# Performance work log

Hardware: AMD Instinct MI355X
Metric: run time of the kernel (lower is better)

## Reference

```python
import jax, jax.numpy as jnp
import numpy as np

B, N, E = 32, 128, 16384
D, H, O, A = 72, 72, 72, 4   # n_input, n_hidden, n_output, n_node_attr
C_WEIGHT = 1.0
EPS = 1e-5  # BatchNorm1d default eps


def setup_inputs() -> dict:
    key = jax.random.key(0)
    ks = jax.random.split(key, 16)
    rn = lambda k, shp, s=0.05: jax.random.normal(k, shp, jnp.float32) * s
    return {
        "h": jax.random.normal(ks[0], (B, N, D), jnp.float32),
        "x": jax.random.normal(ks[1], (B, N, 4), jnp.float32),
        "edgei": jax.random.randint(ks[2], (B, E), 0, N),
        "edgej": jax.random.randint(ks[3], (B, E), 0, N),
        "node_attr": jax.random.normal(ks[4], (B, N, A), jnp.float32),
        # phi_e: Linear(2D+2 -> H, no bias), BN, ReLU, Linear(H->H), ReLU
        "We1": rn(ks[5], (2 * D + 2, H)),
        "g1": jnp.ones((H,), jnp.float32), "b1": jnp.zeros((H,), jnp.float32),
        "We2": rn(ks[6], (H, H)), "be2": jnp.zeros((H,), jnp.float32),
        # phi_m: Linear(H->1), Sigmoid
        "Wm": rn(ks[7], (H, 1)), "bm": jnp.zeros((1,), jnp.float32),
        # phi_x: Linear(H->H), ReLU, Linear(H->1, no bias, tiny init)
        "Wx1": rn(ks[8], (H, H)), "bx1": jnp.zeros((H,), jnp.float32),
        "Wx2": rn(ks[9], (H, 1), 0.001),
        # phi_h: Linear(H+D+A -> H), BN, ReLU, Linear(H->O)
        "Wh1": rn(ks[10], (H + D + A, H)), "bh1": jnp.zeros((H,), jnp.float32),
        "gh": jnp.ones((H,), jnp.float32), "bh": jnp.zeros((H,), jnp.float32),
        "Wh2": rn(ks[11], (H, O)), "bh2": jnp.zeros((O,), jnp.float32),
    }


def _psi(p):
    return jnp.sign(p) * jnp.log1p(jnp.abs(p))


def _normsq4(p):  # Minkowski norm: p0^2 - p1^2 - p2^2 - p3^2
    psq = p * p
    return 2.0 * psq[..., 0] - psq.sum(axis=-1)


def _dotsq4(p, q):  # Minkowski inner product
    pq = p * q
    return 2.0 * pq[..., 0] - pq.sum(axis=-1)


def _batchnorm(z, g, b):  # training-mode BatchNorm1d over flattened batch dim
    mu = z.mean(axis=0)
    var = z.var(axis=0)
    return (z - mu) * jax.lax.rsqrt(var + EPS) * g + b


_seg_sum = jax.vmap(lambda d, s: jax.ops.segment_sum(d, s, num_segments=N))


def reference(h, x, edgei, edgej, node_attr,
              We1, g1, b1, We2, be2, Wm, bm,
              Wx1, bx1, Wx2, Wh1, bh1, gh, bh, Wh2, bh2):
    # gather edge endpoint features (equiv. to torch.gather along dim 1)
    xi = jnp.take_along_axis(x, edgei[:, :, None], axis=1)    # [B,E,4]
    xj = jnp.take_along_axis(x, edgej[:, :, None], axis=1)
    hi = jnp.take_along_axis(h, edgei[:, :, None], axis=1)    # [B,E,D]
    hj = jnp.take_along_axis(h, edgej[:, :, None], axis=1)
    x_diff = xi - xj
    norms = _psi(_normsq4(x_diff))[..., None]                 # [B,E,1]
    dots = _psi(_dotsq4(xi, xj))[..., None]                   # [B,E,1]

    # m_model: phi_e then sigmoid gate phi_m
    feat = jnp.concatenate([hi, hj, norms, dots], axis=-1)    # [B,E,2D+2]
    z = feat.reshape(-1, 2 * D + 2) @ We1
    z = jax.nn.relu(_batchnorm(z, g1, b1))
    z = jax.nn.relu(z @ We2 + be2)
    m = z.reshape(B, E, H)
    m = m * jax.nn.sigmoid(m @ Wm + bm)                       # gated messages

    # x_model: equivariant coordinate update (segment mean over edges)
    gate = jax.nn.relu(m @ Wx1 + bx1) @ Wx2                   # [B,E,1]
    trans = jnp.clip(x_diff * gate, -100.0, 100.0)
    agg = _seg_sum(trans, edgei)                              # [B,N,4]
    cnt = _seg_sum(jnp.ones_like(trans), edgei)
    x_out = x + (agg / jnp.maximum(cnt, 1.0)) * C_WEIGHT

    # h_model: segment sum of messages, node MLP, residual
    magg = _seg_sum(m, edgei)                                 # [B,N,H]
    hin = jnp.concatenate([h, magg, node_attr], axis=-1).reshape(-1, H + D + A)
    z2 = hin @ Wh1 + bh1
    z2 = jax.nn.relu(_batchnorm(z2, gh, bh))
    z2 = z2 @ Wh2 + bh2
    h_out = h + z2.reshape(B, N, O)

    return (h_out, x_out, m)
```

## Files before the change

### kernel.cpp

```cpp
#include <hip/hip_runtime.h>

#define BB 32
#define NN 128
#define EE 16384
#define ROWS_E (BB*EE)
#define ROWS_N (BB*NN)
#define EPS_BN 1e-5f

#define XOUT_OFF (ROWS_N*72)
#define M_OFF    (XOUT_OFF + ROWS_N*4)

#define ST1_OFF 0
#define ST2_OFF 512
#define AGG_OFF 1024
#define CNT_OFF (AGG_OFF + ROWS_N*4)
#define MAGG_OFF (CNT_OFF + ROWS_N)
#define Z2_OFF (MAGG_OFF + ROWS_N*72)
#define ZERO_FLOATS Z2_OFF
#define WB_OFF (Z2_OFF + ROWS_N*72)

#define WE1T_OFF 0
#define WE2T_OFF 13440
#define WX1T_OFF 21760
#define WH1T_OFF 30080
#define WH2T_OFF 43520
#define WB_TOTAL 51840

#define SS 168

typedef __attribute__((ext_vector_type(8))) short short8;
typedef __attribute__((ext_vector_type(4))) float f32x4;

__device__ __forceinline__ float psi_f(float p) {
    return copysignf(log1pf(fabsf(p)), p);
}
__device__ __forceinline__ unsigned pk(float a, float b) {
    unsigned r;
    asm("v_cvt_pk_bf16_f32 %0, %1, %2" : "=v"(r) : "v"(a), "v"(b));
    return r;
}
__device__ __forceinline__ unsigned short f2bf(float f) {
    unsigned r;
    asm("v_cvt_pk_bf16_f32 %0, %1, %1" : "=v"(r) : "v"(f));
    return (unsigned short)r;
}

__global__ void k_prep(const float* __restrict__ We1, const float* __restrict__ We2,
                       const float* __restrict__ Wx1, const float* __restrict__ Wh1,
                       const float* __restrict__ Wh2, unsigned short* __restrict__ wb)
{
    int idx = blockIdx.x * 256 + threadIdx.x;
    if (idx >= WB_TOTAL) return;
    const float* src; int off, n, k, K;
    if (idx < WE2T_OFF)      { off = idx;            n = off/168; k = off%168; src = We1; K = 146; }
    else if (idx < WH1T_OFF && idx >= WX1T_OFF) { off = idx - WX1T_OFF; n = off/104; k = off%104; src = Wx1; K = 72; }
    else if (idx < WX1T_OFF) { off = idx - WE2T_OFF; n = off/104; k = off%104; src = We2; K = 72; }
    else if (idx < WH2T_OFF) { off = idx - WH1T_OFF; n = off/168; k = off%168; src = Wh1; K = 148; }
    else                     { off = idx - WH2T_OFF; n = off/104; k = off%104; src = Wh2; K = 72; }
    float v = (n < 72 && k < K) ? src[k * 72 + n] : 0.f;
    wb[idx] = f2bf(v);
}

__device__ __forceinline__ void stage_feat(
    unsigned short* At, const float* __restrict__ h, const float* __restrict__ x,
    const int* __restrict__ ei, const int* __restrict__ ej, int tid, int blk)
{
    int rl = tid >> 1, half = tid & 1;
    int row = blk * 128 + rl;
    int b = row >> 14;
    int i = ei[row], j = ej[row];
    int node = half ? j : i;
    const float4* hp = (const float4*)(h + (size_t)(b * 128 + node) * 72);
    uint2* arow = (uint2*)(&At[rl * SS + half * 72]);
    #pragma unroll
    for (int q = 0; q < 18; q++) {
        float4 v = hp[q];
        arow[q] = make_uint2(pk(v.x, v.y), pk(v.z, v.w));
    }
    if (half == 0) {
        float4 xi = *(const float4*)(x + (size_t)(b * 128 + i) * 4);
        float4 xj = *(const float4*)(x + (size_t)(b * 128 + j) * 4);
        float d0 = xi.x - xj.x, d1 = xi.y - xj.y, d2 = xi.z - xj.z, d3 = xi.w - xj.w;
        float nrm = d0*d0 - d1*d1 - d2*d2 - d3*d3;
        float dot = xi.x*xj.x - xi.y*xj.y - xi.z*xj.z - xi.w*xj.w;
        *(unsigned*)(&At[rl * SS + 144]) = pk(psi_f(nrm), psi_f(dot));
        unsigned* tp = (unsigned*)(&At[rl * SS + 146]);
        tp[0] = 0u; tp[1] = 0u; tp[2] = 0u;
    } else {
        unsigned* tp = (unsigned*)(&At[rl * SS + 152]);
        tp[0] = 0u; tp[1] = 0u; tp[2] = 0u; tp[3] = 0u;
    }
}

__global__ __launch_bounds__(256, 3) void k_edge_stats(
    const float* __restrict__ h, const float* __restrict__ x,
    const int* __restrict__ ei, const int* __restrict__ ej,
    const unsigned short* __restrict__ We1t, float* __restrict__ st)
{
    __shared__ unsigned short At[128 * SS];
    int tid = threadIdx.x;
    stage_feat(At, h, x, ei, ej, tid, blockIdx.x);

    int wv = tid >> 6, lane = tid & 63, c = lane & 15, quad = lane >> 4;
    f32x4 acc[2][5] = {};
    for (int kc = 0; kc < 5; kc++) {
        int k0 = kc * 32 + quad * 8;
        short8 a0 = *(const short8*)(&At[(wv * 32 + c) * SS + k0]);
        short8 a1 = *(const short8*)(&At[(wv * 32 + 16 + c) * SS + k0]);
        #pragma unroll
        for (int ct = 0; ct < 5; ct++) {
            short8 bf = *(const short8*)(&We1t[(ct * 16 + c) * 168 + k0]);
            acc[0][ct] = __builtin_amdgcn_mfma_f32_16x16x32_bf16(a0, bf, acc[0][ct], 0, 0, 0);
            acc[1][ct] = __builtin_amdgcn_mfma_f32_16x16x32_bf16(a1, bf, acc[1][ct], 0, 0, 0);
        }
    }
    float* sredw = (float*)(&At[wv * 32 * SS]);
    #pragma unroll
    for (int ct = 0; ct < 5; ct++) {
        int col = ct * 16 + c;
        float s = 0.f, q = 0.f;
        #pragma unroll
        for (int rt = 0; rt < 2; rt++)
            #pragma unroll
            for (int r = 0; r < 4; r++) {
                float v = acc[rt][ct][r];
                s += v; q += v * v;
            }
        s += __shfl_xor(s, 16); s += __shfl_xor(s, 32);
        q += __shfl_xor(q, 16); q += __shfl_xor(q, 32);
        if (lane < 16 && col < 72) { sredw[col] = s; sredw[72 + col] = q; }
    }
    __syncthreads();
    if (tid < 144) {
        const float* a = (const float*)At;
        atomicAdd(&st[tid], a[tid] + a[2688 + tid] + a[5376 + tid] + a[8064 + tid]);
    }
}

__global__ void k_finalize(float* __restrict__ st, float inv_rows)
{
    int c = threadIdx.x;
    if (c < 72) {
        float mean = st[c] * inv_rows;
        float var  = st[72 + c] * inv_rows - mean * mean;
        st[144 + c] = mean;
        st[216 + c] = rsqrtf(var + EPS_BN);
    }
}

__global__ __launch_bounds__(256, 3) void k_edge_fused(
    const float* __restrict__ h, const float* __restrict__ x,
    const int* __restrict__ ei, const int* __restrict__ ej,
    const float* __restrict__ st1, const float* __restrict__ g1, const float* __restrict__ b1,
    const float* __restrict__ be2, const float* __restrict__ Wm, const float* __restrict__ bm,
    const float* __restrict__ bx1, const float* __restrict__ Wx2,
    const unsigned short* __restrict__ We1t, const unsigned short* __restrict__ We2t,
    const unsigned short* __restrict__ Wx1t,
    float* __restrict__ m, float* __restrict__ agg, float* __restrict__ cnt)
{
    __shared__ unsigned short At[128 * SS];
    int tid = threadIdx.x;
    stage_feat(At, h, x, ei, ej, tid, blockIdx.x);

    int wv = tid >> 6, lane = tid & 63, c = lane & 15, quad = lane >> 4;
    f32x4 acc1[2][5] = {};
    for (int kc = 0; kc < 5; kc++) {
        int k0 = kc * 32 + quad * 8;
        short8 a0 = *(const short8*)(&At[(wv * 32 + c) * SS + k0]);
        short8 a1 = *(const short8*)(&At[(wv * 32 + 16 + c) * SS + k0]);
        #pragma unroll
        for (int ct = 0; ct < 5; ct++) {
            short8 bf = *(const short8*)(&We1t[(ct * 16 + c) * 168 + k0]);
            acc1[0][ct] = __builtin_amdgcn_mfma_f32_16x16x32_bf16(a0, bf, acc1[0][ct], 0, 0, 0);
            acc1[1][ct] = __builtin_amdgcn_mfma_f32_16x16x32_bf16(a1, bf, acc1[1][ct], 0, 0, 0);
        }
    }
    const float* mean = st1 + 144;
    const float* inv  = st1 + 216;
    #pragma unroll
    for (int ct = 0; ct < 5; ct++) {
        int col = ct * 16 + c;
        float mu = 0.f, iv = 0.f, ga = 0.f, be = 0.f;
        if (col < 72) { mu = mean[col]; iv = inv[col]; ga = g1[col]; be = b1[col]; }
        #pragma unroll
        for (int rt = 0; rt < 2; rt++)
            #pragma unroll
            for (int r = 0; r < 4; r++) {
                float a = (col < 72) ? fmaxf((acc1[rt][ct][r] - mu) * iv * ga + be, 0.f) : 0.f;
                int lrow = wv * 32 + rt * 16 + quad * 4 + r;
                At[lrow * SS + col] = f2bf(a);
            }
    }
    {
        int r_ = lane >> 1, h_ = lane & 1;
        uint* zp = (uint*)&At[(wv * 32 + r_) * SS + 80 + h_ * 8];
        zp[0] = 0u; zp[1] = 0u; zp[2] = 0u; zp[3] = 0u;
    }
    f32x4 acc2[2][5] = {};
    for (int kc = 0; kc < 3; kc++) {
        int k0 = kc * 32 + quad * 8;
        short8 a0 = *(const short8*)(&At[(wv * 32 + c) * SS + k0]);
        short8 a1 = *(const short8*)(&At[(wv * 32 + 16 + c) * SS + k0]);
        #pragma unroll
        for (int ct = 0; ct < 5; ct++) {
            short8 bf = *(const short8*)(&We2t[(ct * 16 + c) * 104 + k0]);
            acc2[0][ct] = __builtin_amdgcn_mfma_f32_16x16x32_bf16(a0, bf, acc2[0][ct], 0, 0, 0);
            acc2[1][ct] = __builtin_amdgcn_mfma_f32_16x16x32_bf16(a1, bf, acc2[1][ct], 0, 0, 0);
        }
    }
    float part[2][4] = {};
    float bm0 = bm[0];
    #pragma unroll
    for (int ct = 0; ct < 5; ct++) {
        int col = ct * 16 + c;
        float bias = (col < 72) ? be2[col] : 0.f;
        float wm   = (col < 72) ? Wm[col]  : 0.f;
        #pragma unroll
        for (int rt = 0; rt < 2; rt++)
            #pragma unroll
            for (int r = 0; r < 4; r++) {
                float t = fmaxf(acc2[rt][ct][r] + bias, 0.f);
                acc2[rt][ct][r] = t;
                part[rt][r] += t * wm;
            }
    }
    float sg[2][4];
    #pragma unroll
    for (int rt = 0; rt < 2; rt++)
        #pragma unroll
        for (int r = 0; r < 4; r++) {
            float s = part[rt][r];
            s += __shfl_xor(s, 1); s += __shfl_xor(s, 2);
            s += __shfl_xor(s, 4); s += __shfl_xor(s, 8);
            sg[rt][r] = 1.f / (1.f + expf(-(s + bm0)));
        }
    size_t rbase = (size_t)blockIdx.x * 128 + wv * 32 + quad * 4;
    #pragma unroll
    for (int rt = 0; rt < 2; rt++)
        #pragma unroll
        for (int ct = 0; ct < 5; ct++) {
            int col = ct * 16 + c;
            #pragma unroll
            for (int r = 0; r < 4; r++) {
                float mv = acc2[rt][ct][r] * sg[rt][r];
                int lrow = wv * 32 + rt * 16 + quad * 4 + r;
                At[lrow * SS + col] = f2bf(mv);
                if (col < 72) m[(rbase + rt * 16 + r) * 72 + col] = mv;
            }
        }
    f32x4 acc3[2][5] = {};
    for (int kc = 0; kc < 3; kc++) {
        int k0 = kc * 32 + quad * 8;
        short8 a0 = *(const short8*)(&At[(wv * 32 + c) * SS + k0]);
        short8 a1 = *(const short8*)(&At[(wv * 32 + 16 + c) * SS + k0]);
        #pragma unroll
        for (int ct = 0; ct < 5; ct++) {
            short8 bf = *(const short8*)(&Wx1t[(ct * 16 + c) * 104 + k0]);
            acc3[0][ct] = __builtin_amdgcn_mfma_f32_16x16x32_bf16(a0, bf, acc3[0][ct], 0, 0, 0);
            acc3[1][ct] = __builtin_amdgcn_mfma_f32_16x16x32_bf16(a1, bf, acc3[1][ct], 0, 0, 0);
        }
    }
    float part3[2][4] = {};
    #pragma unroll
    for (int ct = 0; ct < 5; ct++) {
        int col = ct * 16 + c;
        float bias = (col < 72) ? bx1[col] : 0.f;
        float wx   = (col < 72) ? Wx2[col] : 0.f;
        #pragma unroll
        for (int rt = 0; rt < 2; rt++)
            #pragma unroll
            for (int r = 0; r < 4; r++)
                part3[rt][r] += fmaxf(acc3[rt][ct][r] + bias, 0.f) * wx;
    }
    float* gp = (float*)&At[(wv * 32) * SS + 96];
    #pragma unroll
    for (int rt = 0; rt < 2; rt++)
        #pragma unroll
        for (int r = 0; r < 4; r++) {
            float s = part3[rt][r];
            s += __shfl_xor(s, 1); s += __shfl_xor(s, 2);
            s += __shfl_xor(s, 4); s += __shfl_xor(s, 8);
            if (c == 0) gp[rt * 16 + quad * 4 + r] = s;
        }
    __syncthreads();
    if (tid < 128) {
        size_t erow = (size_t)blockIdx.x * 128 + tid;
        int b = (int)(erow >> 14);
        int i2 = ei[erow], j2 = ej[erow];
        float g2 = *((float*)&At[((tid >> 5) * 32) * SS + 96] + (tid & 31));
        float4 xi = *(const float4*)(x + (size_t)(b * 128 + i2) * 4);
        float4 xj = *(const float4*)(x + (size_t)(b * 128 + j2) * 4);
        float t0 = fminf(fmaxf((xi.x - xj.x) * g2, -100.f), 100.f);
        float t1 = fminf(fmaxf((xi.y - xj.y) * g2, -100.f), 100.f);
        float t2 = fminf(fmaxf((xi.z - xj.z) * g2, -100.f), 100.f);
        float t3 = fminf(fmaxf((xi.w - xj.w) * g2, -100.f), 100.f);
        float* ap = agg + (size_t)(b * 128 + i2) * 4;
        atomicAdd(ap + 0, t0); atomicAdd(ap + 1, t1);
        atomicAdd(ap + 2, t2); atomicAdd(ap + 3, t3);
        atomicAdd(cnt + (size_t)(b * 128 + i2), 1.f);
    }
}

__global__ __launch_bounds__(256, 4) void k_magg(
    const float* __restrict__ m, const int* __restrict__ ei, float* __restrict__ magg)
{
    __shared__ float accum[128 * 72];
    int tid = threadIdx.x;
    for (int q = tid; q < 9216; q += 256) accum[q] = 0.f;
    __syncthreads();
    int b = blockIdx.x >> 5, chunk = blockIdx.x & 31;
    int wv = tid >> 6, lane = tid & 63;
    int ebase = b * 16384 + chunk * 512;
    for (int e = wv; e < 512; e += 8) {
        int e0 = ebase + e, e1 = ebase + e + 4;
        int n0 = ei[e0], n1 = ei[e1];
        const float* r0 = m + (size_t)e0 * 72;
        const float* r1 = m + (size_t)e1 * 72;
        float v0 = r0[lane];
        float v1 = r1[lane];
        float t0 = (lane < 8) ? r0[64 + lane] : 0.f;
        float t1 = (lane < 8) ? r1[64 + lane] : 0.f;
        atomicAdd(&accum[n0 * 72 + lane], v0);
        if (lane < 8) atomicAdd(&accum[n0 * 72 + 64 + lane], t0);
        atomicAdd(&accum[n1 * 72 + lane], v1);
        if (lane < 8) atomicAdd(&accum[n1 * 72 + 64 + lane], t1);
    }
    __syncthreads();
    float* mg = magg + (size_t)b * 9216;
    for (int q = tid; q < 9216; q += 256) atomicAdd(&mg[q], accum[q]);
}

__global__ __launch_bounds__(256) void k_node_gemm1(
    const float* __restrict__ h, const float* __restrict__ node_attr,
    const float* __restrict__ magg, const unsigned short* __restrict__ Wh1t,
    const float* __restrict__ bh1, float* __restrict__ z2, float* __restrict__ st)
{
    __shared__ unsigned short At[128 * 168];
    __shared__ unsigned short Wt[80 * 168];
    __shared__ float sred[4][144];
    int tid = threadIdx.x;
    {
        const uint4* s = (const uint4*)Wh1t; uint4* d = (uint4*)Wt;
        for (int q = tid; q < 1680; q += 256) d[q] = s[q];
    }
    int rl = tid >> 1, half = tid & 1;
    size_t row = (size_t)blockIdx.x * 128 + rl;
    const float4* sp = (const float4*)((half ? magg : h) + row * 72);
    uint2* arow = (uint2*)(&At[rl * 168 + half * 72]);
    #pragma unroll
    for (int q = 0; q < 18; q++) {
        float4 v = sp[q];
        arow[q] = make_uint2(pk(v.x, v.y), pk(v.z, v.w));
    }
    if (half) {
        float4 na = *(const float4*)(node_attr + row * 4);
        *(unsigned*)(&At[rl * 168 + 144]) = pk(na.x, na.y);
        *(unsigned*)(&At[rl * 168 + 146]) = pk(na.z, na.w);
        unsigned* tailp = (unsigned*)(&At[rl * 168 + 148]);
        #pragma unroll
        for (int q = 0; q < 10; q++) tailp[q] = 0u;
    }
    __syncthreads();

    int wv = tid >> 6, lane = tid & 63, c = lane & 15, quad = lane >> 4;
    f32x4 acc[2][5] = {};
    for (int kc = 0; kc < 5; kc++) {
        int k0 = kc * 32 + quad * 8;
        short8 a0 = *(const short8*)(&At[(wv * 32 + c) * 168 + k0]);
        short8 a1 = *(const short8*)(&At[(wv * 32 + 16 + c) * 168 + k0]);
        #pragma unroll
        for (int ct = 0; ct < 5; ct++) {
            short8 bf = *(const short8*)(&Wt[(ct * 16 + c) * 168 + k0]);
            acc[0][ct] = __builtin_amdgcn_mfma_f32_16x16x32_bf16(a0, bf, acc[0][ct], 0, 0, 0);
            acc[1][ct] = __builtin_amdgcn_mfma_f32_16x16x32_bf16(a1, bf, acc[1][ct], 0, 0, 0);
        }
    }
    size_t rbase = (size_t)blockIdx.x * 128 + wv * 32 + quad * 4;
    #pragma unroll
    for (int ct = 0; ct < 5; ct++) {
        int col = ct * 16 + c;
        float bias = (col < 72) ? bh1[col] : 0.f;
        float s = 0.f, q = 0.f;
        #pragma unroll
        for (int rt = 0; rt < 2; rt++) {
            float* op = z2 + (rbase + rt * 16) * 72 + col;
            #pragma unroll
            for (int r = 0; r < 4; r++) {
                float v = acc[rt][ct][r] + bias;
                if (col < 72) op[(size_t)r * 72] = v;
                s += v; q += v * v;
            }
        }
        s += __shfl_xor(s, 16); s += __shfl_xor(s, 32);
        q += __shfl_xor(q, 16); q += __shfl_xor(q, 32);
        if (lane < 16 && col < 72) { sred[wv][col] = s; sred[wv][72 + col] = q; }
    }
    __syncthreads();
    if (tid < 144)
        atomicAdd(&st[tid], sred[0][tid] + sred[1][tid] + sred[2][tid] + sred[3][tid]);
}

__global__ __launch_bounds__(256) void k_node_final(
    const float* __restrict__ h, const float* __restrict__ x,
    const float* __restrict__ z2, const float* __restrict__ st2,
    const float* __restrict__ gh, const float* __restrict__ bh,
    const unsigned short* __restrict__ Wh2t, const float* __restrict__ bh2,
    const float* __restrict__ agg, const float* __restrict__ cnt,
    float* __restrict__ hout, float* __restrict__ xout)
{
    __shared__ unsigned short Zt[128 * 104];
    __shared__ unsigned short Wt[80 * 104];
    int tid = threadIdx.x;
    {
        const uint4* s = (const uint4*)Wh2t; uint4* d = (uint4*)Wt;
        for (int q = tid; q < 1040; q += 256) d[q] = s[q];
    }
    int rl = tid >> 1, half = tid & 1;
    size_t row = (size_t)blockIdx.x * 128 + rl;
    const float* mean = st2 + 144;
    const float* inv  = st2 + 216;
    const float4* zp = (const float4*)(z2 + row * 72) + half * 9;
    uint2* arow = (uint2*)(&Zt[rl * 104 + half * 36]);
    #pragma unroll
    for (int q = 0; q < 9; q++) {
        int k = half * 36 + q * 4;
        float4 v = zp[q];
        float a0 = fmaxf((v.x - mean[k  ]) * inv[k  ] * gh[k  ] + bh[k  ], 0.f);
        float a1 = fmaxf((v.y - mean[k+1]) * inv[k+1] * gh[k+1] + bh[k+1], 0.f);
        float a2 = fmaxf((v.z - mean[k+2]) * inv[k+2] * gh[k+2] + bh[k+2], 0.f);
        float a3 = fmaxf((v.w - mean[k+3]) * inv[k+3] * gh[k+3] + bh[k+3], 0.f);
        arow[q] = make_uint2(pk(a0, a1), pk(a2, a3));
    }
    uint2* prow = (uint2*)(&Zt[rl * 104]);
    #pragma unroll
    for (int q = 0; q < 4; q++) prow[18 + half * 4 + q] = make_uint2(0u, 0u);
    __syncthreads();

    int wv = tid >> 6, lane = tid & 63, c = lane & 15, quad = lane >> 4;
    f32x4 acc[2][5] = {};
    for (int kc = 0; kc < 3; kc++) {
        int k0 = kc * 32 + quad * 8;
        short8 a0 = *(const short8*)(&Zt[(wv * 32 + c) * 104 + k0]);
        short8 a1 = *(const short8*)(&Zt[(wv * 32 + 16 + c) * 104 + k0]);
        #pragma unroll
        for (int ct = 0; ct < 5; ct++) {
            short8 bf = *(const short8*)(&Wt[(ct * 16 + c) * 104 + k0]);
            acc[0][ct] = __builtin_amdgcn_mfma_f32_16x16x32_bf16(a0, bf, acc[0][ct], 0, 0, 0);
            acc[1][ct] = __builtin_amdgcn_mfma_f32_16x16x32_bf16(a1, bf, acc[1][ct], 0, 0, 0);
        }
    }
    size_t rbase = (size_t)blockIdx.x * 128 + wv * 32 + quad * 4;
    #pragma unroll
    for (int rt = 0; rt < 2; rt++)
        #pragma unroll
        for (int ct = 0; ct < 5; ct++) {
            int col = ct * 16 + c;
            if (col < 72) {
                float bias = bh2[col];
                #pragma unroll
                for (int r = 0; r < 4; r++) {
                    size_t gr = (rbase + rt * 16 + r);
                    hout[gr * 72 + col] = h[gr * 72 + col] + acc[rt][ct][r] + bias;
                }
            }
        }
    if (tid < 128) {
        size_t nrow = (size_t)blockIdx.x * 128 + tid;
        float cn = fmaxf(cnt[nrow], 1.f);
        float4 ag = *(const float4*)(agg + nrow * 4);
        float4 xv = *(const float4*)(x + nrow * 4);
        ((float4*)xout)[nrow] = make_float4(xv.x + ag.x / cn, xv.y + ag.y / cn,
                                            xv.z + ag.z / cn, xv.w + ag.w / cn);
    }
}

extern "C" void kernel_launch(void* const* d_in, const int* in_sizes, int n_in,
                              void* d_out, int out_size, void* d_ws, size_t ws_size,
                              hipStream_t stream)
{
    const float* h   = (const float*)d_in[0];
    const float* x   = (const float*)d_in[1];
    const int*   ei  = (const int*)d_in[2];
    const int*   ej  = (const int*)d_in[3];
    const float* na  = (const float*)d_in[4];
    const float* We1 = (const float*)d_in[5];
    const float* g1  = (const float*)d_in[6];
    const float* b1  = (const float*)d_in[7];
    const float* We2 = (const float*)d_in[8];
    const float* be2 = (const float*)d_in[9];
    const float* Wm  = (const float*)d_in[10];
    const float* bm  = (const float*)d_in[11];
    const float* Wx1 = (const float*)d_in[12];
    const float* bx1 = (const float*)d_in[13];
    const float* Wx2 = (const float*)d_in[14];
    const float* Wh1 = (const float*)d_in[15];
    const float* bh1 = (const float*)d_in[16];
    const float* gh  = (const float*)d_in[17];
    const float* bhp = (const float*)d_in[18];
    const float* Wh2 = (const float*)d_in[19];
    const float* bh2 = (const float*)d_in[20];

    float* out  = (float*)d_out;
    float* hout = out;
    float* xout = out + XOUT_OFF;
    float* m    = out + M_OFF;
    float* ws   = (float*)d_ws;
    float* st1  = ws + ST1_OFF;
    float* st2  = ws + ST2_OFF;
    float* agg  = ws + AGG_OFF;
    float* cnt  = ws + CNT_OFF;
    float* magg = ws + MAGG_OFF;
    float* z2   = ws + Z2_OFF;
    unsigned short* wb = (unsigned short*)(ws + WB_OFF);

    hipMemsetAsync(d_ws, 0, (size_t)ZERO_FLOATS * sizeof(float), stream);
    k_prep<<<(WB_TOTAL + 255) / 256, 256, 0, stream>>>(We1, We2, Wx1, Wh1, Wh2, wb);
    k_edge_stats<<<ROWS_E / 128, 256, 0, stream>>>(h, x, ei, ej, wb + WE1T_OFF, st1);
    k_finalize<<<1, 128, 0, stream>>>(st1, 1.0f / (float)ROWS_E);
    k_edge_fused<<<ROWS_E / 128, 256, 0, stream>>>(h, x, ei, ej, st1, g1, b1, be2, Wm, bm,
                                                   bx1, Wx2, wb + WE1T_OFF, wb + WE2T_OFF,
                                                   wb + WX1T_OFF, m, agg, cnt);
    k_magg<<<1024, 256, 0, stream>>>(m, ei, magg);
    k_node_gemm1<<<ROWS_N / 128, 256, 0, stream>>>(h, na, magg, wb + WH1T_OFF, bh1, z2, st2);
    k_finalize<<<1, 128, 0, stream>>>(st2, 1.0f / (float)ROWS_N);
    k_node_final<<<ROWS_N / 128, 256, 0, stream>>>(h, x, z2, st2, gh, bhp,
                                                   wb + WH2T_OFF, bh2, agg, cnt, hout, xout);
}
```

Measured before the change: 700.1 us.

## Factor first edge linear layer into per-node projections gathered per edge

The first edge GEMM over concatenated [hi, hj, norms, dots] is split algebraically into per-node products h@We1[:72] and h@We1[72:144]. These are computed once per node (4096 rows instead of 524288 edges) and gathered per edge with the scalar terms added. The BN statistics pass becomes a lightweight gather-and-reduce kernel instead of a full MFMA pass, and the fused edge kernel skips its first GEMM. BN scale and shift are also prefolded into one multiply-add. It reuses workspace and the x_out buffer as scratch, which adds memset ordering dependencies, and it adds fp32 gathers of 144-wide node rows per edge.

```diff
diff --git a/kernel.cpp b/kernel.cpp
--- a/kernel.cpp
+++ b/kernel.cpp
@@ -16,7 +16,6 @@
 #define CNT_OFF (AGG_OFF + ROWS_N*4)
 #define MAGG_OFF (CNT_OFF + ROWS_N)
 #define Z2_OFF (MAGG_OFF + ROWS_N*72)
-#define ZERO_FLOATS Z2_OFF
 #define WB_OFF (Z2_OFF + ROWS_N*72)
 
 #define WE1T_OFF 0
@@ -25,8 +24,8 @@
 #define WH1T_OFF 30080
 #define WH2T_OFF 43520
 #define WB_TOTAL 51840
-
-#define SS 168
+#define WAB_TOTAL 13824
+#define PREP_TOTAL (WB_TOTAL + WAB_TOTAL)
 
 typedef __attribute__((ext_vector_type(8))) short short8;
 typedef __attribute__((ext_vector_type(4))) float f32x4;
@@ -47,10 +46,18 @@
 
 __global__ void k_prep(const float* __restrict__ We1, const float* __restrict__ We2,
                        const float* __restrict__ Wx1, const float* __restrict__ Wh1,
-                       const float* __restrict__ Wh2, unsigned short* __restrict__ wb)
+                       const float* __restrict__ Wh2, unsigned short* __restrict__ wb,
+                       unsigned short* __restrict__ wab)
 {
     int idx = blockIdx.x * 256 + threadIdx.x;
-    if (idx >= WB_TOTAL) return;
+    if (idx >= PREP_TOTAL) return;
+    if (idx >= WB_TOTAL) {
+        int off = idx - WB_TOTAL, n = off / 96, k = off % 96;
+        float v = 0.f;
+        if (k < 72) v = (n < 72) ? We1[k * 72 + n] : We1[(72 + k) * 72 + (n - 72)];
+        wab[off] = f2bf(v);
+        return;
+    }
     const float* src; int off, n, k, K;
     if (idx < WE2T_OFF)      { off = idx;            n = off/168; k = off%168; src = We1; K = 146; }
     else if (idx < WH1T_OFF && idx >= WX1T_OFF) { off = idx - WX1T_OFF; n = off/104; k = off%104; src = Wx1; K = 72; }
@@ -61,79 +68,94 @@
     wb[idx] = f2bf(v);
 }
 
-__device__ __forceinline__ void stage_feat(
-    unsigned short* At, const float* __restrict__ h, const float* __restrict__ x,
-    const int* __restrict__ ei, const int* __restrict__ ej, int tid, int blk)
-{
+__global__ __launch_bounds__(256, 2) void k_ab(
+    const float* __restrict__ h, const unsigned short* __restrict__ Wabt,
+    float* __restrict__ ab)
+{
+    __shared__ unsigned short Hs[128 * 104];
+    int tid = threadIdx.x;
     int rl = tid >> 1, half = tid & 1;
-    int row = blk * 128 + rl;
-    int b = row >> 14;
-    int i = ei[row], j = ej[row];
-    int node = half ? j : i;
-    const float4* hp = (const float4*)(h + (size_t)(b * 128 + node) * 72);
-    uint2* arow = (uint2*)(&At[rl * SS + half * 72]);
-    #pragma unroll
-    for (int q = 0; q < 18; q++) {
+    size_t row = (size_t)blockIdx.x * 128 + rl;
+    const float4* hp = (const float4*)(h + row * 72) + half * 9;
+    uint2* hr = (uint2*)(&Hs[rl * 104 + half * 36]);
+    #pragma unroll
+    for (int q = 0; q < 9; q++) {
         float4 v = hp[q];
-        arow[q] = make_uint2(pk(v.x, v.y), pk(v.z, v.w));
-    }
-    if (half == 0) {
+        hr[q] = make_uint2(pk(v.x, v.y), pk(v.z, v.w));
+    }
+    {
+        uint2* zp = (uint2*)(&Hs[rl * 104 + 72 + half * 12]);
+        zp[0] = make_uint2(0u, 0u); zp[1] = make_uint2(0u, 0u); zp[2] = make_uint2(0u, 0u);
+    }
+    int wv = tid >> 6, lane = tid & 63, c = lane & 15, quad = lane >> 4;
+    f32x4 acc[2][9] = {};
+    #pragma unroll
+    for (int kc = 0; kc < 3; kc++) {
+        int k0 = kc * 32 + quad * 8;
+        short8 a0 = *(const short8*)(&Hs[(wv * 32 + c) * 104 + k0]);
+        short8 a1 = *(const short8*)(&Hs[(wv * 32 + 16 + c) * 104 + k0]);
+        #pragma unroll
+        for (int ct = 0; ct < 9; ct++) {
+            short8 bf = *(const short8*)(&Wabt[(ct * 16 + c) * 96 + k0]);
+            acc[0][ct] = __builtin_amdgcn_mfma_f32_16x16x32_bf16(a0, bf, acc[0][ct], 0, 0, 0);
+            acc[1][ct] = __builtin_amdgcn_mfma_f32_16x16x32_bf16(a1, bf, acc[1][ct], 0, 0, 0);
+        }
+    }
+    size_t rbase = (size_t)blockIdx.x * 128 + wv * 32 + quad * 4;
+    #pragma unroll
+    for (int rt = 0; rt < 2; rt++)
+        #pragma unroll
+        for (int ct = 0; ct < 9; ct++) {
+            int col = ct * 16 + c;
+            #pragma unroll
+            for (int r = 0; r < 4; r++)
+                ab[(rbase + rt * 16 + r) * 144 + col] = acc[rt][ct][r];
+        }
+}
+
+__global__ void k_stats_lite(
+    const float* __restrict__ ab, const float* __restrict__ x,
+    const int* __restrict__ ei, const int* __restrict__ ej,
+    const float* __restrict__ We1, float* __restrict__ st)
+{
+    __shared__ float ssum[4][72];
+    __shared__ float ssq[4][72];
+    int c = threadIdx.x, ty = threadIdx.y;
+    float al = We1[144 * 72 + c], be = We1[145 * 72 + c];
+    float s = 0.f, q = 0.f;
+    for (int e = blockIdx.x * 4 + ty; e < ROWS_E; e += 4096) {
+        int b = e >> 14;
+        int i = ei[e], j = ej[e];
         float4 xi = *(const float4*)(x + (size_t)(b * 128 + i) * 4);
         float4 xj = *(const float4*)(x + (size_t)(b * 128 + j) * 4);
         float d0 = xi.x - xj.x, d1 = xi.y - xj.y, d2 = xi.z - xj.z, d3 = xi.w - xj.w;
-        float nrm = d0*d0 - d1*d1 - d2*d2 - d3*d3;
-        float dot = xi.x*xj.x - xi.y*xj.y - xi.z*xj.z - xi.w*xj.w;
-        *(unsigned*)(&At[rl * SS + 144]) = pk(psi_f(nrm), psi_f(dot));
-        unsigned* tp = (unsigned*)(&At[rl * SS + 146]);
-        tp[0] = 0u; tp[1] = 0u; tp[2] = 0u;
-    } else {
-        unsigned* tp = (unsigned*)(&At[rl * SS + 152]);
-        tp[0] = 0u; tp[1] = 0u; tp[2] = 0u; tp[3] = 0u;
-    }
-}
-
-__global__ __launch_bounds__(256, 3) void k_edge_stats(
-    const float* __restrict__ h, const float* __restrict__ x,
-    const int* __restrict__ ei, const int* __restrict__ ej,
-    const unsigned short* __restrict__ We1t, float* __restrict__ st)
-{
-    __shared__ unsigned short At[128 * SS];
-    int tid = threadIdx.x;
-    stage_feat(At, h, x, ei, ej, tid, blockIdx.x);
-
-    int wv = tid >> 6, lane = tid & 63, c = lane & 15, quad = lane >> 4;
-    f32x4 acc[2][5] = {};
-    for (int kc = 0; kc < 5; kc++) {
-        int k0 = kc * 32 + quad * 8;
-        short8 a0 = *(const short8*)(&At[(wv * 32 + c) * SS + k0]);
-        short8 a1 = *(const short8*)(&At[(wv * 32 + 16 + c) * SS + k0]);
-        #pragma unroll
-        for (int ct = 0; ct < 5; ct++) {
-            short8 bf = *(const short8*)(&We1t[(ct * 16 + c) * 168 + k0]);
-            acc[0][ct] = __builtin_amdgcn_mfma_f32_16x16x32_bf16(a0, bf, acc[0][ct], 0, 0, 0);
-            acc[1][ct] = __builtin_amdgcn_mfma_f32_16x16x32_bf16(a1, bf, acc[1][ct], 0, 0, 0);
-        }
-    }
-    float* sredw = (float*)(&At[wv * 32 * SS]);
-    #pragma unroll
-    for (int ct = 0; ct < 5; ct++) {
-        int col = ct * 16 + c;
-        float s = 0.f, q = 0.f;
-        #pragma unroll
-        for (int rt = 0; rt < 2; rt++)
-            #pragma unroll
-            for (int r = 0; r < 4; r++) {
-                float v = acc[rt][ct][r];
-                s += v; q += v * v;
-            }
-        s += __shfl_xor(s, 16); s += __shfl_xor(s, 32);
-        q += __shfl_xor(q, 16); q += __shfl_xor(q, 32);
-        if (lane < 16 && col < 72) { sredw[col] = s; sredw[72 + col] = q; }
-    }
-    __syncthreads();
-    if (tid < 144) {
-        const float* a = (const float*)At;
-        atomicAdd(&st[tid], a[tid] + a[2688 + tid] + a[5376 + tid] + a[8064 + tid]);
+        float u = psi_f(d0*d0 - d1*d1 - d2*d2 - d3*d3);
+        float t = psi_f(xi.x*xj.x - xi.y*xj.y - xi.z*xj.z - xi.w*xj.w);
+        float av = ab[(size_t)(b * 128 + i) * 144 + c];
+        float bv = ab[(size_t)(b * 128 + j) * 144 + 72 + c];
+        float z = av + bv + u * al + t * be;
+        s += z; q += z * z;
+    }
+    ssum[ty][c] = s; ssq[ty][c] = q;
+    __syncthreads();
+    if (ty == 0) {
+        s = ssum[0][c] + ssum[1][c] + ssum[2][c] + ssum[3][c];
+        q = ssq[0][c] + ssq[1][c] + ssq[2][c] + ssq[3][c];
+        atomicAdd(&st[c], s);
+        atomicAdd(&st[72 + c], q);
+    }
+}
+
+__global__ void k_finalize1(float* __restrict__ st, const float* __restrict__ g1,
+                            const float* __restrict__ b1, float inv_rows)
+{
+    int c = threadIdx.x;
+    if (c < 72) {
+        float mean = st[c] * inv_rows;
+        float var  = st[72 + c] * inv_rows - mean * mean;
+        float sc = rsqrtf(var + EPS_BN) * g1[c];
+        st[144 + c] = sc;
+        st[216 + c] = b1[c] - mean * sc;
     }
 }
 
@@ -148,59 +170,55 @@
     }
 }
 
-__global__ __launch_bounds__(256, 3) void k_edge_fused(
-    const float* __restrict__ h, const float* __restrict__ x,
+__global__ __launch_bounds__(256, 4) void k_edge_fused(
+    const float* __restrict__ ab, const float* __restrict__ x,
     const int* __restrict__ ei, const int* __restrict__ ej,
-    const float* __restrict__ st1, const float* __restrict__ g1, const float* __restrict__ b1,
+    const float* __restrict__ We1, const float* __restrict__ st1,
     const float* __restrict__ be2, const float* __restrict__ Wm, const float* __restrict__ bm,
     const float* __restrict__ bx1, const float* __restrict__ Wx2,
-    const unsigned short* __restrict__ We1t, const unsigned short* __restrict__ We2t,
-    const unsigned short* __restrict__ Wx1t,
+    const unsigned short* __restrict__ We2t, const unsigned short* __restrict__ Wx1t,
     float* __restrict__ m, float* __restrict__ agg, float* __restrict__ cnt)
 {
-    __shared__ unsigned short At[128 * SS];
+    __shared__ unsigned short Zt[128 * 104];
+    __shared__ float g2buf[128];
     int tid = threadIdx.x;
-    stage_feat(At, h, x, ei, ej, tid, blockIdx.x);
+    int rl = tid >> 1, half = tid & 1;
+    size_t row = (size_t)blockIdx.x * 128 + rl;
+    int b = (int)(row >> 14);
+    int i = ei[row], j = ej[row];
+    float4 xi = *(const float4*)(x + (size_t)(b * 128 + i) * 4);
+    float4 xj = *(const float4*)(x + (size_t)(b * 128 + j) * 4);
+    float d0 = xi.x - xj.x, d1 = xi.y - xj.y, d2 = xi.z - xj.z, d3 = xi.w - xj.w;
+    float u = psi_f(d0*d0 - d1*d1 - d2*d2 - d3*d3);
+    float t = psi_f(xi.x*xj.x - xi.y*xj.y - xi.z*xj.z - xi.w*xj.w);
+    const float4* ar  = (const float4*)(ab + (size_t)(b * 128 + i) * 144 + half * 36);
+    const float4* br  = (const float4*)(ab + (size_t)(b * 128 + j) * 144 + 72 + half * 36);
+    const float4* alp = (const float4*)(We1 + 144 * 72 + half * 36);
+    const float4* bep = (const float4*)(We1 + 145 * 72 + half * 36);
+    const float4* scp = (const float4*)(st1 + 144 + half * 36);
+    const float4* shp = (const float4*)(st1 + 216 + half * 36);
+    uint2* zrow = (uint2*)(&Zt[rl * 104 + half * 36]);
+    #pragma unroll
+    for (int q = 0; q < 9; q++) {
+        float4 av = ar[q], bv = br[q], al = alp[q], be = bep[q], sc = scp[q], sh = shp[q];
+        float z0 = fmaxf((av.x + bv.x + u * al.x + t * be.x) * sc.x + sh.x, 0.f);
+        float z1 = fmaxf((av.y + bv.y + u * al.y + t * be.y) * sc.y + sh.y, 0.f);
+        float z2 = fmaxf((av.z + bv.z + u * al.z + t * be.z) * sc.z + sh.z, 0.f);
+        float z3 = fmaxf((av.w + bv.w + u * al.w + t * be.w) * sc.w + sh.w, 0.f);
+        zrow[q] = make_uint2(pk(z0, z1), pk(z2, z3));
+    }
+    {
+        uint2* zp = (uint2*)(&Zt[rl * 104 + 72 + half * 12]);
+        zp[0] = make_uint2(0u, 0u); zp[1] = make_uint2(0u, 0u); zp[2] = make_uint2(0u, 0u);
+    }
 
     int wv = tid >> 6, lane = tid & 63, c = lane & 15, quad = lane >> 4;
-    f32x4 acc1[2][5] = {};
-    for (int kc = 0; kc < 5; kc++) {
-        int k0 = kc * 32 + quad * 8;
-        short8 a0 = *(const short8*)(&At[(wv * 32 + c) * SS + k0]);
-        short8 a1 = *(const short8*)(&At[(wv * 32 + 16 + c) * SS + k0]);
-        #pragma unroll
-        for (int ct = 0; ct < 5; ct++) {
-            short8 bf = *(const short8*)(&We1t[(ct * 16 + c) * 168 + k0]);
-            acc1[0][ct] = __builtin_amdgcn_mfma_f32_16x16x32_bf16(a0, bf, acc1[0][ct], 0, 0, 0);
-            acc1[1][ct] = __builtin_amdgcn_mfma_f32_16x16x32_bf16(a1, bf, acc1[1][ct], 0, 0, 0);
-        }
-    }
-    const float* mean = st1 + 144;
-    const float* inv  = st1 + 216;
-    #pragma unroll
-    for (int ct = 0; ct < 5; ct++) {
-        int col = ct * 16 + c;
-        float mu = 0.f, iv = 0.f, ga = 0.f, be = 0.f;
-        if (col < 72) { mu = mean[col]; iv = inv[col]; ga = g1[col]; be = b1[col]; }
-        #pragma unroll
-        for (int rt = 0; rt < 2; rt++)
-            #pragma unroll
-            for (int r = 0; r < 4; r++) {
-                float a = (col < 72) ? fmaxf((acc1[rt][ct][r] - mu) * iv * ga + be, 0.f) : 0.f;
-                int lrow = wv * 32 + rt * 16 + quad * 4 + r;
-                At[lrow * SS + col] = f2bf(a);
-            }
-    }
-    {
-        int r_ = lane >> 1, h_ = lane & 1;
-        uint* zp = (uint*)&At[(wv * 32 + r_) * SS + 80 + h_ * 8];
-        zp[0] = 0u; zp[1] = 0u; zp[2] = 0u; zp[3] = 0u;
-    }
     f32x4 acc2[2][5] = {};
+    #pragma unroll
     for (int kc = 0; kc < 3; kc++) {
         int k0 = kc * 32 + quad * 8;
-        short8 a0 = *(const short8*)(&At[(wv * 32 + c) * SS + k0]);
-        short8 a1 = *(const short8*)(&At[(wv * 32 + 16 + c) * SS + k0]);
+        short8 a0 = *(const short8*)(&Zt[(wv * 32 + c) * 104 + k0]);
+        short8 a1 = *(const short8*)(&Zt[(wv * 32 + 16 + c) * 104 + k0]);
         #pragma unroll
         for (int ct = 0; ct < 5; ct++) {
             short8 bf = *(const short8*)(&We2t[(ct * 16 + c) * 104 + k0]);
@@ -219,9 +237,9 @@
         for (int rt = 0; rt < 2; rt++)
             #pragma unroll
             for (int r = 0; r < 4; r++) {
-                float t = fmaxf(acc2[rt][ct][r] + bias, 0.f);
-                acc2[rt][ct][r] = t;
-                part[rt][r] += t * wm;
+                float tv = fmaxf(acc2[rt][ct][r] + bias, 0.f);
+                acc2[rt][ct][r] = tv;
+                part[rt][r] += tv * wm;
             }
     }
     float sg[2][4];
@@ -244,15 +262,16 @@
             for (int r = 0; r < 4; r++) {
                 float mv = acc2[rt][ct][r] * sg[rt][r];
                 int lrow = wv * 32 + rt * 16 + quad * 4 + r;
-                At[lrow * SS + col] = f2bf(mv);
+                Zt[lrow * 104 + col] = f2bf(mv);
                 if (col < 72) m[(rbase + rt * 16 + r) * 72 + col] = mv;
             }
         }
     f32x4 acc3[2][5] = {};
+    #pragma unroll
     for (int kc = 0; kc < 3; kc++) {
         int k0 = kc * 32 + quad * 8;
-        short8 a0 = *(const short8*)(&At[(wv * 32 + c) * SS + k0]);
-        short8 a1 = *(const short8*)(&At[(wv * 32 + 16 + c) * SS + k0]);
+        short8 a0 = *(const short8*)(&Zt[(wv * 32 + c) * 104 + k0]);
+        short8 a1 = *(const short8*)(&Zt[(wv * 32 + 16 + c) * 104 + k0]);
         #pragma unroll
         for (int ct = 0; ct < 5; ct++) {
             short8 bf = *(const short8*)(&Wx1t[(ct * 16 + c) * 104 + k0]);
@@ -272,7 +291,6 @@
             for (int r = 0; r < 4; r++)
                 part3[rt][r] += fmaxf(acc3[rt][ct][r] + bias, 0.f) * wx;
     }
-    float* gp = (float*)&At[(wv * 32) * SS + 96];
     #pragma unroll
     for (int rt = 0; rt < 2; rt++)
         #pragma unroll
@@ -280,24 +298,24 @@
             float s = part3[rt][r];
             s += __shfl_xor(s, 1); s += __shfl_xor(s, 2);
             s += __shfl_xor(s, 4); s += __shfl_xor(s, 8);
-            if (c == 0) gp[rt * 16 + quad * 4 + r] = s;
+            if (c == 0) g2buf[wv * 32 + rt * 16 + quad * 4 + r] = s;
         }
     __syncthreads();
     if (tid < 128) {
         size_t erow = (size_t)blockIdx.x * 128 + tid;
-        int b = (int)(erow >> 14);
+        int b2 = (int)(erow >> 14);
         int i2 = ei[erow], j2 = ej[erow];
-        float g2 = *((float*)&At[((tid >> 5) * 32) * SS + 96] + (tid & 31));
-        float4 xi = *(const float4*)(x + (size_t)(b * 128 + i2) * 4);
-        float4 xj = *(const float4*)(x + (size_t)(b * 128 + j2) * 4);
-        float t0 = fminf(fmaxf((xi.x - xj.x) * g2, -100.f), 100.f);
-        float t1 = fminf(fmaxf((xi.y - xj.y) * g2, -100.f), 100.f);
-        float t2 = fminf(fmaxf((xi.z - xj.z) * g2, -100.f), 100.f);
-        float t3 = fminf(fmaxf((xi.w - xj.w) * g2, -100.f), 100.f);
-        float* ap = agg + (size_t)(b * 128 + i2) * 4;
+        float g2 = g2buf[tid];
+        float4 xi2 = *(const float4*)(x + (size_t)(b2 * 128 + i2) * 4);
+        float4 xj2 = *(const float4*)(x + (size_t)(b2 * 128 + j2) * 4);
+        float t0 = fminf(fmaxf((xi2.x - xj2.x) * g2, -100.f), 100.f);
+        float t1 = fminf(fmaxf((xi2.y - xj2.y) * g2, -100.f), 100.f);
+        float t2 = fminf(fmaxf((xi2.z - xj2.z) * g2, -100.f), 100.f);
+        float t3 = fminf(fmaxf((xi2.w - xj2.w) * g2, -100.f), 100.f);
+        float* ap = agg + (size_t)(b2 * 128 + i2) * 4;
         atomicAdd(ap + 0, t0); atomicAdd(ap + 1, t1);
         atomicAdd(ap + 2, t2); atomicAdd(ap + 3, t3);
-        atomicAdd(cnt + (size_t)(b * 128 + i2), 1.f);
+        atomicAdd(cnt + (size_t)(b2 * 128 + i2), 1.f);
     }
 }
 
@@ -364,6 +382,7 @@
 
     int wv = tid >> 6, lane = tid & 63, c = lane & 15, quad = lane >> 4;
     f32x4 acc[2][5] = {};
+    #pragma unroll
     for (int kc = 0; kc < 5; kc++) {
         int k0 = kc * 32 + quad * 8;
         short8 a0 = *(const short8*)(&At[(wv * 32 + c) * 168 + k0]);
@@ -438,6 +457,7 @@
 
     int wv = tid >> 6, lane = tid & 63, c = lane & 15, quad = lane >> 4;
     f32x4 acc[2][5] = {};
+    #pragma unroll
     for (int kc = 0; kc < 3; kc++) {
         int k0 = kc * 32 + quad * 8;
         short8 a0 = *(const short8*)(&Zt[(wv * 32 + c) * 104 + k0]);
@@ -512,14 +532,18 @@
     float* magg = ws + MAGG_OFF;
     float* z2   = ws + Z2_OFF;
     unsigned short* wb = (unsigned short*)(ws + WB_OFF);
-
-    hipMemsetAsync(d_ws, 0, (size_t)ZERO_FLOATS * sizeof(float), stream);
-    k_prep<<<(WB_TOTAL + 255) / 256, 256, 0, stream>>>(We1, We2, Wx1, Wh1, Wh2, wb);
-    k_edge_stats<<<ROWS_E / 128, 256, 0, stream>>>(h, x, ei, ej, wb + WE1T_OFF, st1);
-    k_finalize<<<1, 128, 0, stream>>>(st1, 1.0f / (float)ROWS_E);
-    k_edge_fused<<<ROWS_E / 128, 256, 0, stream>>>(h, x, ei, ej, st1, g1, b1, be2, Wm, bm,
-                                                   bx1, Wx2, wb + WE1T_OFF, wb + WE2T_OFF,
-                                                   wb + WX1T_OFF, m, agg, cnt);
+    float* ab = ws + MAGG_OFF;
+    unsigned short* wab = (unsigned short*)xout;
+
+    hipMemsetAsync(d_ws, 0, (size_t)MAGG_OFF * sizeof(float), stream);
+    k_prep<<<(PREP_TOTAL + 255) / 256, 256, 0, stream>>>(We1, We2, Wx1, Wh1, Wh2, wb, wab);
+    k_ab<<<ROWS_N / 128, 256, 0, stream>>>(h, wab, ab);
+    k_stats_lite<<<1024, dim3(72, 4), 0, stream>>>(ab, x, ei, ej, We1, st1);
+    k_finalize1<<<1, 128, 0, stream>>>(st1, g1, b1, 1.0f / (float)ROWS_E);
+    k_edge_fused<<<ROWS_E / 128, 256, 0, stream>>>(ab, x, ei, ej, We1, st1, be2, Wm, bm,
+                                                   bx1, Wx2, wb + WE2T_OFF, wb + WX1T_OFF,
+                                                   m, agg, cnt);
+    hipMemsetAsync(magg, 0, (size_t)(ROWS_N * 72) * sizeof(float), stream);
     k_magg<<<1024, 256, 0, stream>>>(m, ei, magg);
     k_node_gemm1<<<ROWS_N / 128, 256, 0, stream>>>(h, na, magg, wb + WH1T_OFF, bh1, z2, st2);
     k_finalize<<<1, 128, 0, stream>>>(st2, 1.0f / (float)ROWS_N);
```

After: 897.9 us. 1.28x slower.
